# Optimization experiments

Hardware: AMD Instinct MI355X
Metric: run time of the kernel (lower is better)

The kernel has to match this reference:

```python
import jax, jax.numpy as jnp
import numpy as np

B, V, C, G, D, H, W, N = 1, 4, 32, 8, 8, 240, 320, 9
EPS = 1e-5  # BatchNorm3d default eps


def grid_sample(img, grid, align_corners, zeros_pad):
    # img [B,C,Hs,Ws], grid [B,Hg,Wg,2] normalized coords; mirrors torch F.grid_sample bilinear
    Bi, Ci, Hs, Ws = img.shape
    gx, gy = grid[..., 0], grid[..., 1]
    if align_corners:
        ix = (gx + 1.0) * 0.5 * (Ws - 1)
        iy = (gy + 1.0) * 0.5 * (Hs - 1)
    else:
        ix = ((gx + 1.0) * Ws - 1.0) * 0.5
        iy = ((gy + 1.0) * Hs - 1.0) * 0.5
    x0 = jnp.floor(ix)
    y0 = jnp.floor(iy)
    wx1 = ix - x0
    wy1 = iy - y0

    def corner(xi, yi, wgt):
        xc = jnp.clip(xi, 0, Ws - 1).astype(jnp.int32)
        yc = jnp.clip(yi, 0, Hs - 1).astype(jnp.int32)
        v = jax.vmap(lambda im, yy, xx: im[:, yy, xx])(img, yc, xc)  # [B,C,Hg,Wg]
        if zeros_pad:
            valid = ((xi >= 0) & (xi <= Ws - 1) & (yi >= 0) & (yi <= Hs - 1)).astype(img.dtype)
            wgt = wgt * valid
        return v * wgt[:, None]

    return (corner(x0, y0, (1 - wx1) * (1 - wy1)) + corner(x0 + 1, y0, wx1 * (1 - wy1))
            + corner(x0, y0 + 1, (1 - wx1) * wy1) + corner(x0 + 1, y0 + 1, wx1 * wy1))


def differentiable_warping(src_fea, src_proj, ref_proj, depth):
    # src_fea [B,Cf,H,W], projs [B,4,4], depth [B,D,H,W] -> [B,Cf,D,H,W]
    Bi, Cf, Hs, Ws = src_fea.shape
    Dd = depth.shape[1]
    proj = src_proj @ jnp.linalg.inv(ref_proj)
    rot, trans = proj[:, :3, :3], proj[:, :3, 3:4]
    yy, xx = jnp.meshgrid(jnp.arange(Hs, dtype=jnp.float32), jnp.arange(Ws, dtype=jnp.float32), indexing='ij')
    xyz = jnp.stack([xx.ravel(), yy.ravel(), jnp.ones(Hs * Ws, jnp.float32)], axis=0)  # [3,HW]
    rot_xyz = jnp.einsum('bij,jk->bik', rot, xyz)  # [B,3,HW]
    pxyz = rot_xyz[:, :, None, :] * depth.reshape(Bi, 1, Dd, Hs * Ws) + trans[:, :, :, None]  # [B,3,D,HW]
    neg = pxyz[:, 2] <= 1e-3
    px = jnp.where(neg, float(Ws), pxyz[:, 0])
    py = jnp.where(neg, float(Hs), pxyz[:, 1])
    pz = jnp.where(neg, 1.0, pxyz[:, 2])
    gx = (px / pz) / ((Ws - 1) / 2.0) - 1.0
    gy = (py / pz) / ((Hs - 1) / 2.0) - 1.0
    grid = jnp.stack([gx, gy], axis=-1).reshape(Bi, Dd * Hs, Ws, 2)
    grid = jax.lax.stop_gradient(grid)  # torch builds the warp grid under no_grad
    warped = grid_sample(src_fea, grid, align_corners=True, zeros_pad=True)  # [B,Cf,D*H,W]
    return warped.reshape(Bi, Cf, Dd, Hs, Ws)


def conv_bn_relu(x, w, bn):
    # 1x1x1 Conv3d (no bias) + BatchNorm3d (inference) + ReLU; x [B,Ci,D,H,W]
    y = jnp.einsum('oi,bidhw->bodhw', w, x)
    g, b, m, v = bn
    s = g / jnp.sqrt(v + EPS)
    return jax.nn.relu(y * s[:, None, None, None] + (b - m * s)[:, None, None, None])


def conv1(x, w, b):
    return jnp.einsum('oi,bidhw->bodhw', w, x) + b[:, None, None, None]


def pixel_wise_net(sim, w0, bn0, w1, bn1, w2, b2):
    y = conv_bn_relu(sim, w0, bn0)
    y = conv_bn_relu(y, w1, bn1)
    y = jax.nn.sigmoid(conv1(y, w2, b2))[:, 0]  # [B,D,H,W]
    return jnp.max(y, axis=1, keepdims=True)  # [B,1,H,W]


def _forward(ref_feature, src_features, ref_proj, src_projs, depth_sample, grid, weight,
             pw_w0, pw_bn0, pw_w1, pw_bn1, pw_w2, pw_b2,
             sn_w0, sn_bn0, sn_w1, sn_bn1, sn_w2, sn_b2):
    Bi, Cf, Hs, Ws = ref_feature.shape
    Gq = pw_w0.shape[1]
    Dd = depth_sample.shape[1]
    ref_g = ref_feature.reshape(Bi, Gq, Cf // Gq, 1, Hs, Ws)
    sim_sum = jnp.zeros((Bi, Gq, Dd, Hs, Ws), jnp.float32)
    w_sum = jnp.zeros((Bi, 1, 1, Hs, Ws), jnp.float32)
    vws = []
    for v in range(src_features.shape[0]):  # small fixed view count
        warped = differentiable_warping(src_features[v], src_projs[v], ref_proj, depth_sample)
        warped = warped.reshape(Bi, Gq, Cf // Gq, Dd, Hs, Ws)
        sim = jnp.mean(warped * ref_g, axis=2)  # [B,G,D,H,W] group correlation
        vw = pixel_wise_net(sim, pw_w0, pw_bn0, pw_w1, pw_bn1, pw_w2, pw_b2)  # [B,1,H,W]
        vws.append(vw)
        sim_sum = sim_sum + sim * vw[:, :, None]
        w_sum = w_sum + vw[:, :, None]
    x = sim_sum / w_sum
    # SimilarityNet: conv stack -> neighbor grid_sample -> adaptive weighted sum
    y = conv_bn_relu(x, sn_w0, sn_bn0)
    y = conv_bn_relu(y, sn_w1, sn_bn1)
    y = conv1(y, sn_w2, sn_b2)[:, 0]  # [B,D,H,W]
    s = grid_sample(y, grid, align_corners=False, zeros_pad=False)  # border pad, [B,D,N*H,W]
    Nn = grid.shape[1] // Hs
    s = s.reshape(Bi, Dd, Nn, Hs, Ws)
    score_vol = jnp.sum(s * weight, axis=2)  # [B,D,H,W]
    score = jax.nn.softmax(score_vol, axis=1)  # exp(log_softmax) == softmax
    depth = jnp.sum(depth_sample * score, axis=1)  # [B,H,W] (is_inverse=False)
    view_weights = jax.lax.stop_gradient(jnp.concatenate(vws, axis=1))  # [B,V,H,W]
    return depth, score, view_weights


def setup_inputs():
    key = jax.random.key(0)
    ks = jax.random.split(key, 20)
    ref_feature = jax.random.normal(ks[0], (B, C, H, W), jnp.float32)
    src_features = jax.random.normal(ks[1], (V, B, C, H, W), jnp.float32)
    f = 500.0
    K = np.array([[f, 0, W / 2.0, 0], [0, f, H / 2.0, 0], [0, 0, 1, 0], [0, 0, 0, 1]], np.float32)
    ref_proj = jnp.asarray(np.tile(K[None], (B, 1, 1)))
    sp = []
    for tx, ty in [(20.0, 0.0), (-20.0, 0.0), (0.0, 10.0), (0.0, -10.0)]:
        E = np.eye(4, dtype=np.float32)
        E[0, 3], E[1, 3] = tx, ty
        sp.append(np.tile((K @ E)[None], (B, 1, 1)))
    src_projs = jnp.asarray(np.stack(sp))
    depth_sample = jnp.sort(425.0 + 510.0 * jax.random.uniform(ks[2], (B, D, H, W), jnp.float32), axis=1)
    # evaluation neighbor grid: per-pixel +-3px learned-style offsets, align_corners=False normalization
    dx = jax.random.uniform(ks[3], (B, N, H, W), minval=-3.0, maxval=3.0)
    dy = jax.random.uniform(ks[4], (B, N, H, W), minval=-3.0, maxval=3.0)
    xs = jnp.arange(W, dtype=jnp.float32)[None, None, None, :]
    ys = jnp.arange(H, dtype=jnp.float32)[None, None, :, None]
    gx = (2.0 * (xs + dx) + 1.0) / W - 1.0
    gy = (2.0 * (ys + dy) + 1.0) / H - 1.0
    grid = jnp.stack([gx, gy], -1).reshape(B, N * H, W, 2)
    weight = jax.random.uniform(ks[5], (B, D, N, H, W), jnp.float32)  # feature*depth weight in (0,1)

    def bn(k, c):
        k1, k2, k3, k4 = jax.random.split(k, 4)
        return jnp.stack([1.0 + 0.1 * jax.random.normal(k1, (c,)), 0.1 * jax.random.normal(k2, (c,)),
                          0.01 * jax.random.normal(k3, (c,)), 1.0 + 0.1 * jax.random.uniform(k4, (c,))])

    return dict(ref_feature=ref_feature, src_features=src_features, ref_proj=ref_proj,
                src_projs=src_projs, depth_sample=depth_sample, grid=grid, weight=weight,
                pw_w0=0.1 * jax.random.normal(ks[6], (16, G)), pw_bn0=bn(ks[7], 16),
                pw_w1=0.1 * jax.random.normal(ks[8], (8, 16)), pw_bn1=bn(ks[9], 8),
                pw_w2=0.1 * jax.random.normal(ks[10], (1, 8)), pw_b2=jnp.zeros((1,), jnp.float32),
                sn_w0=0.1 * jax.random.normal(ks[11], (16, G)), sn_bn0=bn(ks[12], 16),
                sn_w1=0.1 * jax.random.normal(ks[13], (8, 16)), sn_bn1=bn(ks[14], 8),
                sn_w2=0.1 * jax.random.normal(ks[15], (1, 8)), sn_b2=jnp.zeros((1,), jnp.float32))


def reference(ref_feature, src_features, ref_proj, src_projs, depth_sample, grid, weight,
              pw_w0, pw_bn0, pw_w1, pw_bn1, pw_w2, pw_b2,
              sn_w0, sn_bn0, sn_w1, sn_bn1, sn_w2, sn_b2):
    return _forward(ref_feature, src_features, ref_proj, src_projs, depth_sample, grid, weight,
                    pw_w0, pw_bn0, pw_w1, pw_bn1, pw_w2, pw_b2,
                    sn_w0, sn_bn0, sn_w1, sn_bn1, sn_w2, sn_b2)
```

## Files before the change

kernel.cpp:

```cpp
#include <hip/hip_runtime.h>
#include <hip/hip_fp16.h>
#include <cstdint>
#include <cstddef>

#define HH 240
#define WW 320
#define HWPIX 76800
#define NVIEW 4
#define NCH 32
#define NGRP 8
#define NDEP 8
#define NNEI 9
#define SPLANE (HWPIX * NCH)

#define OFF_TAB 64
#define OFF_Y    4096
#define OFF_SRCT 618496
#define OFF_DEPT 6762496

typedef _Float16 h2 __attribute__((ext_vector_type(2)));
typedef __fp16  h8v __attribute__((ext_vector_type(8)));
typedef float f32x16 __attribute__((ext_vector_type(16)));

__device__ __forceinline__ float fdot2_(h2 a, h2 b, float c) {
#if __has_builtin(__builtin_amdgcn_fdot2)
  return __builtin_amdgcn_fdot2(a, b, c, false);
#else
  return c + (float)a.x * (float)b.x + (float)a.y * (float)b.y;
#endif
}
__device__ __forceinline__ h2 pk_(float a, float b) {
#if __has_builtin(__builtin_amdgcn_cvt_pkrtz)
  return __builtin_bit_cast(h2, __builtin_amdgcn_cvt_pkrtz(a, b));
#else
  h2 r; r.x = (_Float16)a; r.y = (_Float16)b; return r;
#endif
}
__device__ __forceinline__ float pkf_(float a, float b) {
  return __builtin_bit_cast(float, pk_(a, b));
}

__device__ __forceinline__ f32x16 mfma_(h8v a, h8v b, f32x16 c) {
  return __builtin_amdgcn_mfma_f32_32x32x16_f16(a, b, c, 0, 0, 0);
}

__device__ __forceinline__ float maxd8(float x) {
  int xi = __builtin_bit_cast(int, x);
  int t = __builtin_amdgcn_mov_dpp(xi, 0xB1, 0xF, 0xF, true);
  x = fmaxf(x, __builtin_bit_cast(float, t));
  xi = __builtin_bit_cast(int, x);
  t = __builtin_amdgcn_mov_dpp(xi, 0x4E, 0xF, 0xF, true);
  x = fmaxf(x, __builtin_bit_cast(float, t));
  xi = __builtin_bit_cast(int, x);
  int a = __builtin_amdgcn_update_dpp(xi, xi, 0x124, 0xF, 0x5, false);
  int b = __builtin_amdgcn_update_dpp(a,  xi, 0x12C, 0xF, 0xA, false);
  x = fmaxf(x, __builtin_bit_cast(float, b));
  return x;
}

__device__ __forceinline__ float mlp_mfma(float4 x4, h8v w0f, h8v w1f,
                                          float4 b1s, float4 w2s, float b2v,
                                          bool lo) {
  f32x16 Z = {};
  float4 xsw;
  xsw.x = __shfl_xor(x4.x, 32, 64);
  xsw.y = __shfl_xor(x4.y, 32, 64);
  xsw.z = __shfl_xor(x4.z, 32, 64);
  xsw.w = __shfl_xor(x4.w, 32, 64);
  float4 cst;
  cst.x = __builtin_bit_cast(float, 0x00003C00u);
  cst.y = 0.0f; cst.z = 0.0f; cst.w = 0.0f;
  float4 blo, bhi;
  blo.x = lo ? x4.x : cst.x;  blo.y = lo ? x4.y : cst.y;
  blo.z = lo ? x4.z : cst.z;  blo.w = lo ? x4.w : cst.w;
  bhi.x = lo ? xsw.x : cst.x; bhi.y = lo ? xsw.y : cst.y;
  bhi.z = lo ? xsw.z : cst.z; bhi.w = lo ? xsw.w : cst.w;

  float yv0 = 0.0f, yv1 = 0.0f;
#pragma unroll
  for (int bb = 0; bb < 2; ++bb) {
    float4 bin = bb ? bhi : blo;
    f32x16 acc = mfma_(w0f, __builtin_bit_cast(h8v, bin), Z);
    float dw0 = pkf_(fmaxf(acc[0], 0.f), fmaxf(acc[1], 0.f));
    float dw1 = pkf_(fmaxf(acc[2], 0.f), fmaxf(acc[3], 0.f));
    float dw2 = pkf_(fmaxf(acc[4], 0.f), fmaxf(acc[5], 0.f));
    float dw3 = pkf_(fmaxf(acc[6], 0.f), fmaxf(acc[7], 0.f));
    float s0 = __shfl_xor(dw0, 32, 64);
    float s1 = __shfl_xor(dw1, 32, 64);
    float s2 = __shfl_xor(dw2, 32, 64);
    float s3 = __shfl_xor(dw3, 32, 64);
    float4 bf;
    bf.x = lo ? dw0 : s2;
    bf.y = lo ? dw1 : s3;
    bf.z = lo ? s0 : dw2;
    bf.w = lo ? s1 : dw3;
    f32x16 a2 = mfma_(w1f, __builtin_bit_cast(h8v, bf), Z);
    float p = fmaxf(a2[0] + b1s.x, 0.f) * w2s.x;
    p = fmaf(fmaxf(a2[1] + b1s.y, 0.f), w2s.y, p);
    p = fmaf(fmaxf(a2[2] + b1s.z, 0.f), w2s.z, p);
    p = fmaf(fmaxf(a2[3] + b1s.w, 0.f), w2s.w, p);
    p += __shfl_xor(p, 32, 64);
    if (bb) yv1 = p + b2v; else yv0 = p + b2v;
  }
  return lo ? yv0 : yv1;
}

__global__ __launch_bounds__(256) void k_prep(
    const float* __restrict__ src, const float* __restrict__ ref,
    const float* __restrict__ depthS,
    __half* __restrict__ dst, float* __restrict__ dep_t,
    const float* __restrict__ refP, const float* __restrict__ srcP,
    const float* __restrict__ pw0, const float* __restrict__ pbn0,
    const float* __restrict__ pw1, const float* __restrict__ pbn1,
    const float* __restrict__ pw2, const float* __restrict__ pb2,
    const float* __restrict__ sw0, const float* __restrict__ sbn0,
    const float* __restrict__ sw1, const float* __restrict__ sbn1,
    const float* __restrict__ sw2, const float* __restrict__ sb2,
    float* __restrict__ ws, int nTransBlocks) {
  if ((int)blockIdx.x == nTransBlocks) {
    int tid = threadIdx.x;
    if (tid < 128) {
      int net = tid >> 6;
      int l = tid & 63;
      int n = l & 31;
      int hi = l >> 5;
      const float* W0 = net ? sw0 : pw0;  const float* B0 = net ? sbn0 : pbn0;
      const float* W1 = net ? sw1 : pw1;  const float* B1 = net ? sbn1 : pbn1;
      const float* W2 = net ? sw2 : pw2;
      float* base = ws + OFF_TAB + net * 1024;
      float4 r;
      if (hi == 0 && n < 16) {
        float s = B0[n] / sqrtf(B0[48 + n] + 1e-5f) * 0.25f;
        r.x = pkf_(W0[n * 8 + 0] * s, W0[n * 8 + 1] * s);
        r.y = pkf_(W0[n * 8 + 2] * s, W0[n * 8 + 3] * s);
        r.z = pkf_(W0[n * 8 + 4] * s, W0[n * 8 + 5] * s);
        r.w = pkf_(W0[n * 8 + 6] * s, W0[n * 8 + 7] * s);
      } else if (hi == 1 && n < 16) {
        float s = B0[n] / sqrtf(B0[48 + n] + 1e-5f);
        float b0f = B0[16 + n] - B0[32 + n] * s;
        r.x = pkf_(b0f, 0.f); r.y = 0.f; r.z = 0.f; r.w = 0.f;
      } else { r.x = r.y = r.z = r.w = 0.f; }
      ((float4*)(base))[l] = r;
      float4 q;
      if (n < 8) {
        float s = B1[n] / sqrtf(B1[24 + n] + 1e-5f);
        int o = n * 16 + 8 * hi;
        q.x = pkf_(W1[o + 0] * s, W1[o + 1] * s);
        q.y = pkf_(W1[o + 2] * s, W1[o + 3] * s);
        q.z = pkf_(W1[o + 4] * s, W1[o + 5] * s);
        q.w = pkf_(W1[o + 6] * s, W1[o + 7] * s);
      } else { q.x = q.y = q.z = q.w = 0.f; }
      ((float4*)(base + 256))[l] = q;
      float4 b;
      {
        float bb[4];
        for (int rr = 0; rr < 4; ++rr) {
          int o = rr + 4 * hi;
          float s = B1[o] / sqrtf(B1[24 + o] + 1e-5f);
          bb[rr] = B1[8 + o] - B1[16 + o] * s;
        }
        b.x = bb[0]; b.y = bb[1]; b.z = bb[2]; b.w = bb[3];
      }
      ((float4*)(base + 512))[l] = b;
      float4 w2v;
      w2v.x = W2[0 + 4 * hi]; w2v.y = W2[1 + 4 * hi];
      w2v.z = W2[2 + 4 * hi]; w2v.w = W2[3 + 4 * hi];
      ((float4*)(base + 768))[l] = w2v;
    } else if (tid == 128) {
      ws[62] = pb2[0];
      ws[63] = sb2[0];
    } else if (tid == 129) {
      float a[4][8];
      for (int i = 0; i < 4; ++i)
        for (int j = 0; j < 4; ++j) { a[i][j] = refP[i * 4 + j]; a[i][4 + j] = (i == j) ? 1.0f : 0.0f; }
      for (int c = 0; c < 4; ++c) {
        int piv = c; float best = fabsf(a[c][c]);
        for (int r2 = c + 1; r2 < 4; ++r2) { float t = fabsf(a[r2][c]); if (t > best) { best = t; piv = r2; } }
        if (piv != c) for (int j = 0; j < 8; ++j) { float t = a[c][j]; a[c][j] = a[piv][j]; a[piv][j] = t; }
        float inv = 1.0f / a[c][c];
        for (int j = 0; j < 8; ++j) a[c][j] *= inv;
        for (int r2 = 0; r2 < 4; ++r2) if (r2 != c) {
          float f = a[r2][c];
          for (int j = 0; j < 8; ++j) a[r2][j] -= f * a[c][j];
        }
      }
      for (int v = 0; v < NVIEW; ++v) {
        const float* S = srcP + v * 16;
        for (int i = 0; i < 3; ++i)
          for (int j = 0; j < 4; ++j) {
            float p = S[i*4+0]*a[0][4+j] + S[i*4+1]*a[1][4+j] + S[i*4+2]*a[2][4+j] + S[i*4+3]*a[3][4+j];
            if (j < 3) ws[v * 12 + i * 3 + j] = p;
            else       ws[v * 12 + 9 + i] = p;
          }
      }
    }
    return;
  }
  int t = blockIdx.x * 256 + threadIdx.x;
  const int base = 5 * HWPIX * 4;
  if (t >= base) {
    int pix = t - base;
    float4 a, b;
    a.x = depthS[0 * HWPIX + pix]; a.y = depthS[1 * HWPIX + pix];
    a.z = depthS[2 * HWPIX + pix]; a.w = depthS[3 * HWPIX + pix];
    b.x = depthS[4 * HWPIX + pix]; b.y = depthS[5 * HWPIX + pix];
    b.z = depthS[6 * HWPIX + pix]; b.w = depthS[7 * HWPIX + pix];
    float4* o = reinterpret_cast<float4*>(dep_t + (size_t)pix * NDEP);
    o[0] = a; o[1] = b;
    return;
  }
  int c8 = t & 3;
  int vp = t >> 2;
  int v = vp / HWPIX;
  int pix = vp - v * HWPIX;
  const float* s = (v < NVIEW) ? (src + ((size_t)(v * NCH + c8 * 8)) * HWPIX + pix)
                               : (ref + ((size_t)(c8 * 8)) * HWPIX + pix);
  union { h2 h[4]; float4 f; } u;
  u.h[0] = pk_(s[0],         s[HWPIX]);
  u.h[1] = pk_(s[2 * HWPIX], s[3 * HWPIX]);
  u.h[2] = pk_(s[4 * HWPIX], s[5 * HWPIX]);
  u.h[3] = pk_(s[6 * HWPIX], s[7 * HWPIX]);
  reinterpret_cast<float4*>(dst + (size_t)vp * NCH)[c8] = u.f;
}

__device__ __forceinline__ void tap_f16(const __half* __restrict__ p, float wtf,
                                        h2 wp[16], bool first) {
  _Float16 wh = (_Float16)wtf;
  h2 wt2 = h2{wh, wh};
  const float4* q = reinterpret_cast<const float4*>(p);
#pragma unroll
  for (int i = 0; i < 4; ++i) {
    union { float4 f; h2 h[4]; } u; u.f = q[i];
#pragma unroll
    for (int c = 0; c < 4; ++c) {
      if (first) wp[4 * i + c] = u.h[c] * wt2;
      else       wp[4 * i + c] += u.h[c] * wt2;
    }
  }
}

__global__ __launch_bounds__(256) void k_main(
    const __half* __restrict__ srcT, const float* __restrict__ dep_t,
    const float* __restrict__ wsc,
    float* __restrict__ ybuf, float* __restrict__ outVW) {
  int t = blockIdx.x * 256 + threadIdx.x;
  int lane = threadIdx.x & 63;
  bool lo = lane < 32;
  int d = t & 7;
  int pix = t >> 3;
  int h = pix / WW;
  int w = pix - h * WW;
  float fx = (float)w, fy = (float)h;

  const h8v* Tw0p = (const h8v*)(wsc + OFF_TAB);
  const h8v* Tw1p = (const h8v*)(wsc + OFF_TAB + 256);
  h8v w0f_pw = Tw0p[lane];
  h8v w1f_pw = Tw1p[lane];
  float4 b1s_pw = ((const float4*)(wsc + OFF_TAB + 512))[lane];
  float4 w2s_pw = ((const float4*)(wsc + OFF_TAB + 768))[lane];
  float b2_pw = wsc[62];

  h2 rc[16];
  {
    const float4* rp = reinterpret_cast<const float4*>(srcT + (size_t)NVIEW * SPLANE + (size_t)pix * NCH);
#pragma unroll
    for (int i = 0; i < 4; ++i) {
      union { float4 f; h2 h[4]; } u; u.f = rp[i];
      rc[4*i] = u.h[0]; rc[4*i+1] = u.h[1]; rc[4*i+2] = u.h[2]; rc[4*i+3] = u.h[3];
    }
  }
  float dep = dep_t[(size_t)pix * NDEP + d];

  float ssum[NGRP];
#pragma unroll
  for (int g = 0; g < NGRP; ++g) ssum[g] = 0.0f;
  float wsum = 0.0f;

#pragma unroll 1
  for (int v = 0; v < NVIEW; ++v) {
    const float* pr = wsc + v * 12;
    float rx = fmaf(pr[0], fx, fmaf(pr[1], fy, pr[2]));
    float ry = fmaf(pr[3], fx, fmaf(pr[4], fy, pr[5]));
    float rz = fmaf(pr[6], fx, fmaf(pr[7], fy, pr[8]));
    float pz_ = fmaf(rz, dep, pr[11]);
    bool neg = (pz_ <= 0.001f);
    float px_ = neg ? (float)WW : fmaf(rx, dep, pr[9]);
    float py_ = neg ? (float)HH : fmaf(ry, dep, pr[10]);
    float rpz = neg ? 1.0f : __fdividef(1.0f, pz_);
    float ix = px_ * rpz;
    float iy = py_ * rpz;
    float x0f = floorf(ix), y0f = floorf(iy);
    float wx1 = ix - x0f, wy1 = iy - y0f;
    float wx0 = 1.0f - wx1, wy0 = 1.0f - wy1;
    float x1f = x0f + 1.0f, y1f = y0f + 1.0f;
    float vx0 = (x0f >= 0.0f && x0f <= (float)(WW - 1)) ? 1.0f : 0.0f;
    float vx1 = (x1f >= 0.0f && x1f <= (float)(WW - 1)) ? 1.0f : 0.0f;
    float vy0 = (y0f >= 0.0f && y0f <= (float)(HH - 1)) ? 1.0f : 0.0f;
    float vy1 = (y1f >= 0.0f && y1f <= (float)(HH - 1)) ? 1.0f : 0.0f;
    int xa = (int)fminf(fmaxf(x0f, 0.0f), (float)(WW - 1));
    int xb = (int)fminf(fmaxf(x1f, 0.0f), (float)(WW - 1));
    int ya = (int)fminf(fmaxf(y0f, 0.0f), (float)(HH - 1));
    int yb = (int)fminf(fmaxf(y1f, 0.0f), (float)(HH - 1));
    float w00 = wx0 * wy0 * vx0 * vy0;
    float w01 = wx1 * wy0 * vx1 * vy0;
    float w10 = wx0 * wy1 * vx0 * vy1;
    float w11 = wx1 * wy1 * vx1 * vy1;

    float simf[NGRP];
    {
      const __half* vbase = srcT + (size_t)v * SPLANE;
      h2 wp[16];
      tap_f16(vbase + (size_t)(ya * WW + xa) * NCH, w00, wp, true);
      tap_f16(vbase + (size_t)(ya * WW + xb) * NCH, w01, wp, false);
      tap_f16(vbase + (size_t)(yb * WW + xa) * NCH, w10, wp, false);
      tap_f16(vbase + (size_t)(yb * WW + xb) * NCH, w11, wp, false);
#pragma unroll
      for (int g = 0; g < NGRP; ++g)
        simf[g] = fdot2_(wp[2*g+1], rc[2*g+1], fdot2_(wp[2*g], rc[2*g], 0.0f));
    }

    float4 xp;
    xp.x = pkf_(simf[0], simf[1]);
    xp.y = pkf_(simf[2], simf[3]);
    xp.z = pkf_(simf[4], simf[5]);
    xp.w = pkf_(simf[6], simf[7]);
    float sc = mlp_mfma(xp, w0f_pw, w1f_pw, b1s_pw, w2s_pw, b2_pw, lo);
    sc = maxd8(sc);
    float vw = __fdividef(1.0f, 1.0f + __expf(-sc));
#pragma unroll
    for (int g = 0; g < NGRP; ++g) ssum[g] = fmaf(simf[g], vw, ssum[g]);
    wsum += vw;
    if (d == 0) outVW[v * HWPIX + pix] = vw;
  }

  float rw = __fdividef(1.0f, wsum);
  float4 xg;
  xg.x = pkf_(ssum[0] * rw, ssum[1] * rw);
  xg.y = pkf_(ssum[2] * rw, ssum[3] * rw);
  xg.z = pkf_(ssum[4] * rw, ssum[5] * rw);
  xg.w = pkf_(ssum[6] * rw, ssum[7] * rw);
  h8v w0f_sn = ((const h8v*)(wsc + OFF_TAB + 1024))[lane];
  h8v w1f_sn = ((const h8v*)(wsc + OFF_TAB + 1024 + 256))[lane];
  float4 b1s_sn = ((const float4*)(wsc + OFF_TAB + 1024 + 512))[lane];
  float4 w2s_sn = ((const float4*)(wsc + OFF_TAB + 1024 + 768))[lane];
  float b2_sn = wsc[63];
  float yv = mlp_mfma(xg, w0f_sn, w1f_sn, b1s_sn, w2s_sn, b2_sn, lo);
  ybuf[pix * NDEP + d] = yv;
}

__global__ __launch_bounds__(256) void k_score(
    const float* __restrict__ grid, const float* __restrict__ weight,
    const float* __restrict__ dep_t, const float* __restrict__ ybuf,
    float* __restrict__ out) {
  int pix = blockIdx.x * 256 + threadIdx.x;
  int h = pix / WW;
  int w = pix - h * WW;
  float sv[NDEP];
#pragma unroll
  for (int d = 0; d < NDEP; ++d) sv[d] = 0.0f;

#pragma unroll 1
  for (int n = 0; n < NNEI; ++n) {
    int gi = ((n * HH + h) * WW + w) * 2;
    float gx = grid[gi], gy = grid[gi + 1];
    float ix = ((gx + 1.0f) * (float)WW - 1.0f) * 0.5f;
    float iy = ((gy + 1.0f) * (float)HH - 1.0f) * 0.5f;
    float x0f = floorf(ix), y0f = floorf(iy);
    float wx1 = ix - x0f, wy1 = iy - y0f;
    float wx0 = 1.0f - wx1, wy0 = 1.0f - wy1;
    int xa = (int)fminf(fmaxf(x0f, 0.0f), (float)(WW - 1));
    int xb = (int)fminf(fmaxf(x0f + 1.0f, 0.0f), (float)(WW - 1));
    int ya = (int)fminf(fmaxf(y0f, 0.0f), (float)(HH - 1));
    int yb2 = (int)fminf(fmaxf(y0f + 1.0f, 0.0f), (float)(HH - 1));
    const float4* p00 = reinterpret_cast<const float4*>(ybuf + (size_t)(ya * WW + xa) * NDEP);
    const float4* p01 = reinterpret_cast<const float4*>(ybuf + (size_t)(ya * WW + xb) * NDEP);
    const float4* p10 = reinterpret_cast<const float4*>(ybuf + (size_t)(yb2 * WW + xa) * NDEP);
    const float4* p11 = reinterpret_cast<const float4*>(ybuf + (size_t)(yb2 * WW + xb) * NDEP);
    float4 a00 = p00[0], b00 = p00[1];
    float4 a01 = p01[0], b01 = p01[1];
    float4 a10 = p10[0], b10 = p10[1];
    float4 a11 = p11[0], b11 = p11[1];
    const float* v00 = (const float*)&a00;
    const float* v01 = (const float*)&a01;
    const float* v10 = (const float*)&a10;
    const float* v11 = (const float*)&a11;
    const float* u00 = (const float*)&b00;
    const float* u01 = (const float*)&b01;
    const float* u10 = (const float*)&b10;
    const float* u11 = (const float*)&b11;
#pragma unroll
    for (int d = 0; d < NDEP; ++d) {
      float c00 = (d < 4) ? v00[d] : u00[d - 4];
      float c01 = (d < 4) ? v01[d] : u01[d - 4];
      float c10 = (d < 4) ? v10[d] : u10[d - 4];
      float c11 = (d < 4) ? v11[d] : u11[d - 4];
      float s = wy0 * fmaf(wx0, c00, wx1 * c01) + wy1 * fmaf(wx0, c10, wx1 * c11);
      float wn = weight[((size_t)(d * NNEI + n) * HH + h) * WW + w];
      sv[d] = fmaf(s, wn, sv[d]);
    }
  }
  float m = sv[0];
#pragma unroll
  for (int d = 1; d < NDEP; ++d) m = fmaxf(m, sv[d]);
  float e[NDEP], s8 = 0.0f;
#pragma unroll
  for (int d = 0; d < NDEP; ++d) { e[d] = __expf(sv[d] - m); s8 += e[d]; }
  float r = __fdividef(1.0f, s8);
  const float4* dp4 = reinterpret_cast<const float4*>(dep_t + (size_t)pix * NDEP);
  float4 da = dp4[0], db = dp4[1];
  float dpv[NDEP] = {da.x, da.y, da.z, da.w, db.x, db.y, db.z, db.w};
  float dp = 0.0f;
#pragma unroll
  for (int d = 0; d < NDEP; ++d) {
    float sc = e[d] * r;
    out[HWPIX + d * HWPIX + pix] = sc;
    dp = fmaf(dpv[d], sc, dp);
  }
  out[pix] = dp;
}

extern "C" void kernel_launch(void* const* d_in, const int* in_sizes, int n_in,
                              void* d_out, int out_size, void* d_ws, size_t ws_size,
                              hipStream_t stream) {
  const float* ref    = (const float*)d_in[0];
  const float* src    = (const float*)d_in[1];
  const float* refP   = (const float*)d_in[2];
  const float* srcP   = (const float*)d_in[3];
  const float* depthS = (const float*)d_in[4];
  const float* grid   = (const float*)d_in[5];
  const float* weight = (const float*)d_in[6];
  float* out = (float*)d_out;
  float* ws  = (float*)d_ws;
  __half* srcT = (__half*)(ws + OFF_SRCT);
  float* dep_t = ws + OFF_DEPT;

  int transThreads = 5 * HWPIX * 4 + HWPIX;
  int nTransBlocks = transThreads / 256;

  k_prep<<<nTransBlocks + 1, 256, 0, stream>>>(
      src, ref, depthS, srcT, dep_t, refP, srcP,
      (const float*)d_in[7],  (const float*)d_in[8],
      (const float*)d_in[9],  (const float*)d_in[10],
      (const float*)d_in[11], (const float*)d_in[12],
      (const float*)d_in[13], (const float*)d_in[14],
      (const float*)d_in[15], (const float*)d_in[16],
      (const float*)d_in[17], (const float*)d_in[18],
      ws, nTransBlocks);
  k_main<<<(HWPIX * 8) / 256, 256, 0, stream>>>(srcT, dep_t, ws, ws + OFF_Y, out + 9 * HWPIX);
  k_score<<<HWPIX / 256, 256, 0, stream>>>(grid, weight, dep_t, ws + OFF_Y, out);
}
```

Before: 89.82 us.

## Split channel quarters across four lanes per pixel-depth in main kernel

Each (pixel, depth) pair is now handled by four lanes, each lane owning 8 of the 32 channels. Each lane loads one float4 per bilinear tap instead of four, and computes two group similarities. The eight group values are reassembled across lanes with DPP quad permutes before the MFMA MLP. The reductions are reworked for the new lane mapping and the grid is four times larger. This aims to raise parallelism and cut per-thread registers and load latency, at the cost of redundant projection math, extra cross-lane shuffles, and four times more MLP MFMA work, since every lane still runs it.

Result: slower. 115.3 us (+28.3%).

```diff
diff --git a/kernel.cpp b/kernel.cpp
--- a/kernel.cpp
+++ b/kernel.cpp
@@ -44,18 +44,38 @@
   return __builtin_amdgcn_mfma_f32_32x32x16_f16(a, b, c, 0, 0, 0);
 }
 
-__device__ __forceinline__ float maxd8(float x) {
+template <int CTRL>
+__device__ __forceinline__ float dppf(float x) {
   int xi = __builtin_bit_cast(int, x);
-  int t = __builtin_amdgcn_mov_dpp(xi, 0xB1, 0xF, 0xF, true);
-  x = fmaxf(x, __builtin_bit_cast(float, t));
-  xi = __builtin_bit_cast(int, x);
-  t = __builtin_amdgcn_mov_dpp(xi, 0x4E, 0xF, 0xF, true);
-  x = fmaxf(x, __builtin_bit_cast(float, t));
-  xi = __builtin_bit_cast(int, x);
+  return __builtin_bit_cast(float, __builtin_amdgcn_mov_dpp(xi, CTRL, 0xF, 0xF, true));
+}
+
+__device__ __forceinline__ float maxd8v2(float x) {
+  int xi = __builtin_bit_cast(int, x);
   int a = __builtin_amdgcn_update_dpp(xi, xi, 0x124, 0xF, 0x5, false);
   int b = __builtin_amdgcn_update_dpp(a,  xi, 0x12C, 0xF, 0xA, false);
   x = fmaxf(x, __builtin_bit_cast(float, b));
+  x = fmaxf(x, dppf<0x128>(x));
+  x = fmaxf(x, __shfl_xor(x, 16, 64));
   return x;
+}
+
+__device__ __forceinline__ float pick4(float a, float b, float c, float e, int m) {
+  float t01 = (m & 1) ? b : a;
+  float t23 = (m & 1) ? e : c;
+  return (m & 2) ? t23 : t01;
+}
+
+__device__ __forceinline__ float4 qgather(float xi, int chq) {
+  float b = dppf<0xB1>(xi);
+  float c = dppf<0x4E>(xi);
+  float e = dppf<0x1B>(xi);
+  float4 r;
+  r.x = pick4(xi, b, c, e, chq);
+  r.y = pick4(xi, b, c, e, chq ^ 1);
+  r.z = pick4(xi, b, c, e, chq ^ 2);
+  r.w = pick4(xi, b, c, e, chq ^ 3);
+  return r;
 }
 
 __device__ __forceinline__ float mlp_mfma(float4 x4, h8v w0f, h8v w1f,
@@ -223,19 +243,16 @@
   reinterpret_cast<float4*>(dst + (size_t)vp * NCH)[c8] = u.f;
 }
 
-__device__ __forceinline__ void tap_f16(const __half* __restrict__ p, float wtf,
-                                        h2 wp[16], bool first) {
+__device__ __forceinline__ void tap4(const __half* __restrict__ p, float wtf,
+                                     h2 wp[4], bool first) {
   _Float16 wh = (_Float16)wtf;
   h2 wt2 = h2{wh, wh};
-  const float4* q = reinterpret_cast<const float4*>(p);
-#pragma unroll
-  for (int i = 0; i < 4; ++i) {
-    union { float4 f; h2 h[4]; } u; u.f = q[i];
-#pragma unroll
-    for (int c = 0; c < 4; ++c) {
-      if (first) wp[4 * i + c] = u.h[c] * wt2;
-      else       wp[4 * i + c] += u.h[c] * wt2;
-    }
+  union { float4 f; h2 h[4]; } u;
+  u.f = *reinterpret_cast<const float4*>(p);
+#pragma unroll
+  for (int c = 0; c < 4; ++c) {
+    if (first) wp[c] = u.h[c] * wt2;
+    else       wp[c] += u.h[c] * wt2;
   }
 }
 
@@ -243,37 +260,31 @@
     const __half* __restrict__ srcT, const float* __restrict__ dep_t,
     const float* __restrict__ wsc,
     float* __restrict__ ybuf, float* __restrict__ outVW) {
-  int t = blockIdx.x * 256 + threadIdx.x;
-  int lane = threadIdx.x & 63;
+  int tid = threadIdx.x;
+  int lane = tid & 63;
+  int chq = lane & 3;
+  int d = (lane >> 2) & 7;
   bool lo = lane < 32;
-  int d = t & 7;
-  int pix = t >> 3;
+  int pix = blockIdx.x * 8 + (tid >> 5);
   int h = pix / WW;
   int w = pix - h * WW;
   float fx = (float)w, fy = (float)h;
 
-  const h8v* Tw0p = (const h8v*)(wsc + OFF_TAB);
-  const h8v* Tw1p = (const h8v*)(wsc + OFF_TAB + 256);
-  h8v w0f_pw = Tw0p[lane];
-  h8v w1f_pw = Tw1p[lane];
+  h8v w0f_pw = ((const h8v*)(wsc + OFF_TAB))[lane];
+  h8v w1f_pw = ((const h8v*)(wsc + OFF_TAB + 256))[lane];
   float4 b1s_pw = ((const float4*)(wsc + OFF_TAB + 512))[lane];
   float4 w2s_pw = ((const float4*)(wsc + OFF_TAB + 768))[lane];
   float b2_pw = wsc[62];
 
-  h2 rc[16];
+  h2 rc0, rc1, rc2, rc3;
   {
-    const float4* rp = reinterpret_cast<const float4*>(srcT + (size_t)NVIEW * SPLANE + (size_t)pix * NCH);
-#pragma unroll
-    for (int i = 0; i < 4; ++i) {
-      union { float4 f; h2 h[4]; } u; u.f = rp[i];
-      rc[4*i] = u.h[0]; rc[4*i+1] = u.h[1]; rc[4*i+2] = u.h[2]; rc[4*i+3] = u.h[3];
-    }
+    union { float4 f; h2 h[4]; } u;
+    u.f = *reinterpret_cast<const float4*>(srcT + (size_t)NVIEW * SPLANE + (size_t)pix * NCH + chq * 8);
+    rc0 = u.h[0]; rc1 = u.h[1]; rc2 = u.h[2]; rc3 = u.h[3];
   }
   float dep = dep_t[(size_t)pix * NDEP + d];
 
-  float ssum[NGRP];
-#pragma unroll
-  for (int g = 0; g < NGRP; ++g) ssum[g] = 0.0f;
+  float ssumA = 0.0f, ssumB = 0.0f;
   float wsum = 0.0f;
 
 #pragma unroll 1
@@ -306,46 +317,37 @@
     float w10 = wx0 * wy1 * vx0 * vy1;
     float w11 = wx1 * wy1 * vx1 * vy1;
 
-    float simf[NGRP];
+    float simA, simB;
     {
-      const __half* vbase = srcT + (size_t)v * SPLANE;
-      h2 wp[16];
-      tap_f16(vbase + (size_t)(ya * WW + xa) * NCH, w00, wp, true);
-      tap_f16(vbase + (size_t)(ya * WW + xb) * NCH, w01, wp, false);
-      tap_f16(vbase + (size_t)(yb * WW + xa) * NCH, w10, wp, false);
-      tap_f16(vbase + (size_t)(yb * WW + xb) * NCH, w11, wp, false);
-#pragma unroll
-      for (int g = 0; g < NGRP; ++g)
-        simf[g] = fdot2_(wp[2*g+1], rc[2*g+1], fdot2_(wp[2*g], rc[2*g], 0.0f));
+      const __half* vbase = srcT + (size_t)v * SPLANE + chq * 8;
+      h2 wp[4];
+      tap4(vbase + (size_t)(ya * WW + xa) * NCH, w00, wp, true);
+      tap4(vbase + (size_t)(ya * WW + xb) * NCH, w01, wp, false);
+      tap4(vbase + (size_t)(yb * WW + xa) * NCH, w10, wp, false);
+      tap4(vbase + (size_t)(yb * WW + xb) * NCH, w11, wp, false);
+      simA = fdot2_(wp[1], rc1, fdot2_(wp[0], rc0, 0.0f));
+      simB = fdot2_(wp[3], rc3, fdot2_(wp[2], rc2, 0.0f));
     }
 
-    float4 xp;
-    xp.x = pkf_(simf[0], simf[1]);
-    xp.y = pkf_(simf[2], simf[3]);
-    xp.z = pkf_(simf[4], simf[5]);
-    xp.w = pkf_(simf[6], simf[7]);
+    float4 xp = qgather(pkf_(simA, simB), chq);
     float sc = mlp_mfma(xp, w0f_pw, w1f_pw, b1s_pw, w2s_pw, b2_pw, lo);
-    sc = maxd8(sc);
+    sc = maxd8v2(sc);
     float vw = __fdividef(1.0f, 1.0f + __expf(-sc));
-#pragma unroll
-    for (int g = 0; g < NGRP; ++g) ssum[g] = fmaf(simf[g], vw, ssum[g]);
+    ssumA = fmaf(simA, vw, ssumA);
+    ssumB = fmaf(simB, vw, ssumB);
     wsum += vw;
-    if (d == 0) outVW[v * HWPIX + pix] = vw;
+    if ((lane & 31) == 0) outVW[v * HWPIX + pix] = vw;
   }
 
   float rw = __fdividef(1.0f, wsum);
-  float4 xg;
-  xg.x = pkf_(ssum[0] * rw, ssum[1] * rw);
-  xg.y = pkf_(ssum[2] * rw, ssum[3] * rw);
-  xg.z = pkf_(ssum[4] * rw, ssum[5] * rw);
-  xg.w = pkf_(ssum[6] * rw, ssum[7] * rw);
+  float4 xg = qgather(pkf_(ssumA * rw, ssumB * rw), chq);
   h8v w0f_sn = ((const h8v*)(wsc + OFF_TAB + 1024))[lane];
   h8v w1f_sn = ((const h8v*)(wsc + OFF_TAB + 1024 + 256))[lane];
   float4 b1s_sn = ((const float4*)(wsc + OFF_TAB + 1024 + 512))[lane];
   float4 w2s_sn = ((const float4*)(wsc + OFF_TAB + 1024 + 768))[lane];
   float b2_sn = wsc[63];
   float yv = mlp_mfma(xg, w0f_sn, w1f_sn, b1s_sn, w2s_sn, b2_sn, lo);
-  ybuf[pix * NDEP + d] = yv;
+  if (chq == 0) ybuf[pix * NDEP + d] = yv;
 }
 
 __global__ __launch_bounds__(256) void k_score(
@@ -446,6 +448,6 @@
       (const float*)d_in[15], (const float*)d_in[16],
       (const float*)d_in[17], (const float*)d_in[18],
       ws, nTransBlocks);
-  k_main<<<(HWPIX * 8) / 256, 256, 0, stream>>>(srcT, dep_t, ws, ws + OFF_Y, out + 9 * HWPIX);
+  k_main<<<HWPIX / 8, 256, 0, stream>>>(srcT, dep_t, ws, ws + OFF_Y, out + 9 * HWPIX);
   k_score<<<HWPIX / 256, 256, 0, stream>>>(grid, weight, dep_t, ws + OFF_Y, out);
 }
```

## Split source features into channel-quarter planes and map depth across warps

Applied to the files above, without the earlier changes.

The fp16 transposed source layout changes from 32 channels per pixel to four planes of 8 channels each. k_main is remapped so each warp covers 64 consecutive pixels at one depth, with 8 warps per block covering the 8 depths. Neighbouring lanes then gather adjacent 16-byte chunks, which should coalesce the bilinear taps better. The max over depths, previously a DPP reduction within the wavefront, now goes through shared memory with two __syncthreads per view, adding barrier overhead. Depth is read directly from the input instead of the transposed copy.

Result: faster. 84.08 us (-6.4%).

```diff
diff --git a/kernel.cpp b/kernel.cpp
--- a/kernel.cpp
+++ b/kernel.cpp
@@ -11,7 +11,7 @@
 #define NGRP 8
 #define NDEP 8
 #define NNEI 9
-#define SPLANE (HWPIX * NCH)
+#define QPLANE (HWPIX * 8)
 
 #define OFF_TAB 64
 #define OFF_Y    4096
@@ -42,20 +42,6 @@
 
 __device__ __forceinline__ f32x16 mfma_(h8v a, h8v b, f32x16 c) {
   return __builtin_amdgcn_mfma_f32_32x32x16_f16(a, b, c, 0, 0, 0);
-}
-
-__device__ __forceinline__ float maxd8(float x) {
-  int xi = __builtin_bit_cast(int, x);
-  int t = __builtin_amdgcn_mov_dpp(xi, 0xB1, 0xF, 0xF, true);
-  x = fmaxf(x, __builtin_bit_cast(float, t));
-  xi = __builtin_bit_cast(int, x);
-  t = __builtin_amdgcn_mov_dpp(xi, 0x4E, 0xF, 0xF, true);
-  x = fmaxf(x, __builtin_bit_cast(float, t));
-  xi = __builtin_bit_cast(int, x);
-  int a = __builtin_amdgcn_update_dpp(xi, xi, 0x124, 0xF, 0x5, false);
-  int b = __builtin_amdgcn_update_dpp(a,  xi, 0x12C, 0xF, 0xA, false);
-  x = fmaxf(x, __builtin_bit_cast(float, b));
-  return x;
 }
 
 __device__ __forceinline__ float mlp_mfma(float4 x4, h8v w0f, h8v w1f,
@@ -197,7 +183,7 @@
     return;
   }
   int t = blockIdx.x * 256 + threadIdx.x;
-  const int base = 5 * HWPIX * 4;
+  const int base = 20 * HWPIX;
   if (t >= base) {
     int pix = t - base;
     float4 a, b;
@@ -209,67 +195,64 @@
     o[0] = a; o[1] = b;
     return;
   }
-  int c8 = t & 3;
-  int vp = t >> 2;
-  int v = vp / HWPIX;
-  int pix = vp - v * HWPIX;
-  const float* s = (v < NVIEW) ? (src + ((size_t)(v * NCH + c8 * 8)) * HWPIX + pix)
-                               : (ref + ((size_t)(c8 * 8)) * HWPIX + pix);
+  int vq = t / HWPIX;
+  int pix = t - vq * HWPIX;
+  int v = vq >> 2;
+  int q = vq & 3;
+  const float* s = (v < NVIEW) ? (src + ((size_t)(v * NCH + q * 8)) * HWPIX + pix)
+                               : (ref + ((size_t)(q * 8)) * HWPIX + pix);
   union { h2 h[4]; float4 f; } u;
   u.h[0] = pk_(s[0],         s[HWPIX]);
   u.h[1] = pk_(s[2 * HWPIX], s[3 * HWPIX]);
   u.h[2] = pk_(s[4 * HWPIX], s[5 * HWPIX]);
   u.h[3] = pk_(s[6 * HWPIX], s[7 * HWPIX]);
-  reinterpret_cast<float4*>(dst + (size_t)vp * NCH)[c8] = u.f;
-}
-
-__device__ __forceinline__ void tap_f16(const __half* __restrict__ p, float wtf,
-                                        h2 wp[16], bool first) {
+  reinterpret_cast<float4*>(dst + (size_t)vq * QPLANE)[pix] = u.f;
+}
+
+__device__ __forceinline__ void tapq(const __half* __restrict__ p, float wtf,
+                                     h2* __restrict__ wp, bool first) {
   _Float16 wh = (_Float16)wtf;
   h2 wt2 = h2{wh, wh};
-  const float4* q = reinterpret_cast<const float4*>(p);
-#pragma unroll
-  for (int i = 0; i < 4; ++i) {
-    union { float4 f; h2 h[4]; } u; u.f = q[i];
-#pragma unroll
-    for (int c = 0; c < 4; ++c) {
-      if (first) wp[4 * i + c] = u.h[c] * wt2;
-      else       wp[4 * i + c] += u.h[c] * wt2;
-    }
-  }
-}
-
-__global__ __launch_bounds__(256) void k_main(
-    const __half* __restrict__ srcT, const float* __restrict__ dep_t,
+  union { float4 f; h2 h[4]; } u;
+  u.f = *reinterpret_cast<const float4*>(p);
+#pragma unroll
+  for (int c = 0; c < 4; ++c) {
+    if (first) wp[c] = u.h[c] * wt2;
+    else       wp[c] += u.h[c] * wt2;
+  }
+}
+
+__global__ __launch_bounds__(512) void k_main(
+    const __half* __restrict__ srcT, const float* __restrict__ depthS,
     const float* __restrict__ wsc,
     float* __restrict__ ybuf, float* __restrict__ outVW) {
-  int t = blockIdx.x * 256 + threadIdx.x;
-  int lane = threadIdx.x & 63;
+  __shared__ float sred[NDEP * 64];
+  int tid = threadIdx.x;
+  int lane = tid & 63;
+  int d = tid >> 6;
   bool lo = lane < 32;
-  int d = t & 7;
-  int pix = t >> 3;
+  int pix = blockIdx.x * 64 + lane;
   int h = pix / WW;
   int w = pix - h * WW;
   float fx = (float)w, fy = (float)h;
 
-  const h8v* Tw0p = (const h8v*)(wsc + OFF_TAB);
-  const h8v* Tw1p = (const h8v*)(wsc + OFF_TAB + 256);
-  h8v w0f_pw = Tw0p[lane];
-  h8v w1f_pw = Tw1p[lane];
+  h8v w0f_pw = ((const h8v*)(wsc + OFF_TAB))[lane];
+  h8v w1f_pw = ((const h8v*)(wsc + OFF_TAB + 256))[lane];
   float4 b1s_pw = ((const float4*)(wsc + OFF_TAB + 512))[lane];
   float4 w2s_pw = ((const float4*)(wsc + OFF_TAB + 768))[lane];
   float b2_pw = wsc[62];
 
   h2 rc[16];
   {
-    const float4* rp = reinterpret_cast<const float4*>(srcT + (size_t)NVIEW * SPLANE + (size_t)pix * NCH);
-#pragma unroll
-    for (int i = 0; i < 4; ++i) {
-      union { float4 f; h2 h[4]; } u; u.f = rp[i];
-      rc[4*i] = u.h[0]; rc[4*i+1] = u.h[1]; rc[4*i+2] = u.h[2]; rc[4*i+3] = u.h[3];
+    const __half* refb = srcT + (size_t)16 * QPLANE;
+#pragma unroll
+    for (int q = 0; q < 4; ++q) {
+      union { float4 f; h2 hh[4]; } u;
+      u.f = *reinterpret_cast<const float4*>(refb + (size_t)q * QPLANE + (size_t)pix * 8);
+      rc[4*q] = u.hh[0]; rc[4*q+1] = u.hh[1]; rc[4*q+2] = u.hh[2]; rc[4*q+3] = u.hh[3];
     }
   }
-  float dep = dep_t[(size_t)pix * NDEP + d];
+  float dep = depthS[d * HWPIX + pix];
 
   float ssum[NGRP];
 #pragma unroll
@@ -306,14 +289,21 @@
     float w10 = wx0 * wy1 * vx0 * vy1;
     float w11 = wx1 * wy1 * vx1 * vy1;
 
+    int t00 = ya * WW + xa, t01 = ya * WW + xb;
+    int t10 = yb * WW + xa, t11 = yb * WW + xb;
+
     float simf[NGRP];
     {
-      const __half* vbase = srcT + (size_t)v * SPLANE;
+      const __half* vb = srcT + (size_t)(v * 4) * QPLANE;
       h2 wp[16];
-      tap_f16(vbase + (size_t)(ya * WW + xa) * NCH, w00, wp, true);
-      tap_f16(vbase + (size_t)(ya * WW + xb) * NCH, w01, wp, false);
-      tap_f16(vbase + (size_t)(yb * WW + xa) * NCH, w10, wp, false);
-      tap_f16(vbase + (size_t)(yb * WW + xb) * NCH, w11, wp, false);
+#pragma unroll
+      for (int q = 0; q < 4; ++q) {
+        const __half* pb = vb + (size_t)q * QPLANE;
+        tapq(pb + (size_t)t00 * 8, w00, wp + 4 * q, true);
+        tapq(pb + (size_t)t01 * 8, w01, wp + 4 * q, false);
+        tapq(pb + (size_t)t10 * 8, w10, wp + 4 * q, false);
+        tapq(pb + (size_t)t11 * 8, w11, wp + 4 * q, false);
+      }
 #pragma unroll
       for (int g = 0; g < NGRP; ++g)
         simf[g] = fdot2_(wp[2*g+1], rc[2*g+1], fdot2_(wp[2*g], rc[2*g], 0.0f));
@@ -325,8 +315,15 @@
     xp.z = pkf_(simf[4], simf[5]);
     xp.w = pkf_(simf[6], simf[7]);
     float sc = mlp_mfma(xp, w0f_pw, w1f_pw, b1s_pw, w2s_pw, b2_pw, lo);
-    sc = maxd8(sc);
-    float vw = __fdividef(1.0f, 1.0f + __expf(-sc));
+
+    sred[(d << 6) | lane] = sc;
+    __syncthreads();
+    float m = sred[lane];
+#pragma unroll
+    for (int j = 1; j < NDEP; ++j) m = fmaxf(m, sred[(j << 6) | lane]);
+    __syncthreads();
+    float vw = __fdividef(1.0f, 1.0f + __expf(-m));
+
 #pragma unroll
     for (int g = 0; g < NGRP; ++g) ssum[g] = fmaf(simf[g], vw, ssum[g]);
     wsum += vw;
@@ -434,7 +431,7 @@
   __half* srcT = (__half*)(ws + OFF_SRCT);
   float* dep_t = ws + OFF_DEPT;
 
-  int transThreads = 5 * HWPIX * 4 + HWPIX;
+  int transThreads = 20 * HWPIX + HWPIX;
   int nTransBlocks = transThreads / 256;
 
   k_prep<<<nTransBlocks + 1, 256, 0, stream>>>(
@@ -446,6 +443,6 @@
       (const float*)d_in[15], (const float*)d_in[16],
       (const float*)d_in[17], (const float*)d_in[18],
       ws, nTransBlocks);
-  k_main<<<(HWPIX * 8) / 256, 256, 0, stream>>>(srcT, dep_t, ws, ws + OFF_Y, out + 9 * HWPIX);
+  k_main<<<HWPIX / 64, 512, 0, stream>>>(srcT, depthS, ws, ws + OFF_Y, out + 9 * HWPIX);
   k_score<<<HWPIX / 256, 256, 0, stream>>>(grid, weight, dep_t, ws + OFF_Y, out);
 }
```
